# Performance work log

Measured on AMD Instinct MI355X. Metric: run time of the kernel, lower is better.

The kernel has to match this reference:

```python
import jax, jax.numpy as jnp
import numpy as np

EMBED_DIM = 1024
NUM_HEADS = 16
HEAD_DIM = EMBED_DIM // NUM_HEADS
SCALE = HEAD_DIM ** -0.5


def setup_inputs() -> dict:
    key = jax.random.key(0)
    k1, k2, k3 = jax.random.split(key, 3)
    B, S, E = 2, 2048, EMBED_DIM
    # xavier-uniform-like init scaled down for stability
    x = jax.random.normal(k1, (B, S, E), dtype=jnp.float32)
    w_qkv = jax.random.normal(k2, (3 * E, E), dtype=jnp.float32) * (E ** -0.5)
    w_out = jax.random.normal(k3, (E, E), dtype=jnp.float32) * (E ** -0.5)
    bias_qkv = jnp.zeros((3 * E,), dtype=jnp.float32)
    bias_out = jnp.zeros((E,), dtype=jnp.float32)
    return {"x": x, "w_qkv": w_qkv, "bias_qkv": bias_qkv, "w_out": w_out, "bias_out": bias_out}


def reference(x, w_qkv, bias_qkv, w_out, bias_out):
    B, S, E = x.shape
    H, D = NUM_HEADS, HEAD_DIM
    # fused QKV projection: nn.Linear semantics -> x @ w_qkv.T + bias
    qkv = jnp.einsum('bse,fe->bsf', x, w_qkv) + bias_qkv  # [B,S,3E]
    q, k, v = jnp.split(qkv, 3, axis=-1)
    # reshape to heads
    q = q.reshape(B, S, H, D)
    k = k.reshape(B, S, H, D)
    v = v.reshape(B, S, H, D)
    # scaled dot-product attention (non-causal)
    scores = jnp.einsum('bqhd,bkhd->bhqk', q, k) * SCALE  # [B,H,S,S]
    probs = jax.nn.softmax(scores, axis=-1)
    ctx = jnp.einsum('bhqk,bkhd->bqhd', probs, v).reshape(B, S, E)
    # output projection
    out = jnp.einsum('bse,fe->bsf', ctx, w_out) + bias_out
    return out
```

## Files before the change

kernel.cpp:

```cpp
#include <hip/hip_runtime.h>
#include <hip/hip_bf16.h>


typedef __bf16 bf16_t;
typedef __bf16 bf16x4 __attribute__((ext_vector_type(4)));
typedef __bf16 bf16x8 __attribute__((ext_vector_type(8)));
typedef float f32x4 __attribute__((ext_vector_type(4)));

#define MFMA16(a, b, c) __builtin_amdgcn_mfma_f32_16x16x32_bf16(a, b, c, 0, 0, 0)

static constexpr int Bn = 2;
static constexpr int S = 2048;
static constexpr int E = 1024;
static constexpr int H = 16;
static constexpr int Dh = 64;

__device__ __forceinline__ void gl_lds16(const bf16_t* g, bf16_t* l) {
  __builtin_amdgcn_global_load_lds(
      (const __attribute__((address_space(1))) unsigned int*)g,
      (__attribute__((address_space(3))) unsigned int*)l, 16, 0, 0);
}

__device__ __forceinline__ int detect_fp32(const unsigned short* p) {
  int cnt = 0;
#pragma unroll
  for (int j = 0; j < 32; j++) {
    const int e = (p[j] >> 7) & 0xFF;
    cnt += (e > 140) ? 1 : 0;
  }
  return cnt >= 2;
}

static constexpr int G0 = 4194304 / 8;
static constexpr int G1 = G0 + 3145728 / 8;
static constexpr int G2 = G1 + 3072 / 8;
static constexpr int G3 = G2 + 1048576 / 8;
static constexpr int G4 = G3 + 1024 / 8;

__global__ void convert_all(const void* __restrict__ s0, const void* __restrict__ s1,
                            const void* __restrict__ s2, const void* __restrict__ s3,
                            const void* __restrict__ s4, bf16_t* __restrict__ dst) {
  const int fp32 = detect_fp32((const unsigned short*)s0);
  const int stride = gridDim.x * blockDim.x;
  for (int i = blockIdx.x * blockDim.x + threadIdx.x; i < G4; i += stride) {
    const void* s;
    int off;
    if (i < G0)      { s = s0; off = i; }
    else if (i < G1) { s = s1; off = i - G0; }
    else if (i < G2) { s = s2; off = i - G1; }
    else if (i < G3) { s = s3; off = i - G2; }
    else             { s = s4; off = i - G3; }
    bf16x8 o;
    if (fp32) {
      const float* sp = (const float*)s + off * 8;
#pragma unroll
      for (int j = 0; j < 8; j++) o[j] = (bf16_t)sp[j];
    } else {
      o = *((const bf16x8*)s + off);
    }
    *(bf16x8*)(dst + (size_t)i * 8) = o;
  }
}

__global__ __launch_bounds__(256) void gemm_qkv(
    const bf16_t* __restrict__ X, const bf16_t* __restrict__ W,
    const bf16_t* __restrict__ bias,
    bf16_t* __restrict__ Qo, bf16_t* __restrict__ Ko, bf16_t* __restrict__ Vo) {
  __shared__ bf16_t Alds[16 * 512];
  __shared__ bf16_t Blds[16 * 512];
  const int tid = threadIdx.x;
  const int wave = tid >> 6, lane = tid & 63;
  const int lr = lane & 15, quad = lane >> 4;
  const int wm = wave >> 1, wn = wave & 1;
  const int m0 = blockIdx.y * 128, n0 = blockIdx.x * 128;
  constexpr int Kd = 1024;

  f32x4 acc[4][4] = {};
  for (int k0 = 0; k0 < Kd; k0 += 64) {
    __syncthreads();
#pragma unroll
    for (int i = 0; i < 4; i++) {
      const int fb = wave * 4 + i;
      const int mt = fb >> 1, kc = fb & 1;
      gl_lds16(X + (size_t)(m0 + mt * 16 + lr) * Kd + k0 + kc * 32 + quad * 8,
               &Alds[fb * 512]);
      gl_lds16(W + (size_t)(n0 + mt * 16 + lr) * Kd + k0 + kc * 32 + quad * 8,
               &Blds[fb * 512]);
    }
    __syncthreads();
#pragma unroll
    for (int kc = 0; kc < 2; kc++) {
      bf16x8 af[4], bfr[4];
#pragma unroll
      for (int mt = 0; mt < 4; mt++)
        af[mt] = *(const bf16x8*)&Alds[((wm * 4 + mt) * 2 + kc) * 512 + lane * 8];
#pragma unroll
      for (int nt = 0; nt < 4; nt++)
        bfr[nt] = *(const bf16x8*)&Blds[((wn * 4 + nt) * 2 + kc) * 512 + lane * 8];
#pragma unroll
      for (int mt = 0; mt < 4; mt++)
#pragma unroll
        for (int nt = 0; nt < 4; nt++)
          acc[mt][nt] = MFMA16(af[mt], bfr[nt], acc[mt][nt]);
    }
  }

  const int m0w = m0 + wm * 64, n0w = n0 + wn * 64;
#pragma unroll
  for (int nt = 0; nt < 4; nt++) {
    const int col = n0w + nt * 16 + lr;
    const float bs = (float)bias[col];
    const int which = col >> 10;
    const int e = col & 1023;
    const int h = e >> 6, d = e & 63;
#pragma unroll
    for (int mt = 0; mt < 4; mt++) {
      const int row0 = m0w + mt * 16 + quad * 4;
      const int b = row0 >> 11, s0 = row0 & 2047;
      if (which == 2) {
        bf16x4 v4;
#pragma unroll
        for (int r = 0; r < 4; r++) v4[r] = (bf16_t)(acc[mt][nt][r] + bs);
        *(bf16x4*)&Vo[((size_t)((b * H + h) * Dh + d)) * S + s0] = v4;
      } else {
        bf16_t* dst = (which == 0) ? Qo : Ko;
#pragma unroll
        for (int r = 0; r < 4; r++)
          dst[((size_t)((b * H + h) * S + (s0 + r))) * Dh + d] =
              (bf16_t)(acc[mt][nt][r] + bs);
      }
    }
  }
}

__global__ __launch_bounds__(256, 2) void attn_kernel(
    const bf16_t* __restrict__ Q, const bf16_t* __restrict__ K,
    const bf16_t* __restrict__ Vt, bf16_t* __restrict__ CTX) {
  __shared__ bf16_t Kl[2 * 8 * 512];
  __shared__ bf16_t Vl[2 * 8 * 512];
  __shared__ bf16_t Psh[4 * 32 * 64];

  const int tid = threadIdx.x;
  const int wave = tid >> 6, lane = tid & 63;
  const int lr = lane & 15, quad = lane >> 4;

  const int blk = blockIdx.x;
  const int bh = blk & 31;
  const int qt = blk >> 5;
  const int b = bh >> 4, h = bh & 15;

  const bf16_t* Qb = Q + (size_t)bh * S * Dh;
  const bf16_t* Kb = K + (size_t)bh * S * Dh;
  const bf16_t* Vb = Vt + (size_t)bh * Dh * S;

  const int q0 = qt * 128 + wave * 32;

  bf16x8 aq[2][2];
#pragma unroll
  for (int mt = 0; mt < 2; mt++)
#pragma unroll
    for (int kc = 0; kc < 2; kc++) {
      bf16x8 t = *(const bf16x8*)(Qb + (size_t)(q0 + mt * 16 + lr) * Dh +
                                  kc * 32 + quad * 8);
#pragma unroll
      for (int j = 0; j < 8; j++) t[j] = (bf16_t)((float)t[j] * 0.125f);
      aq[mt][kc] = t;
    }

  bf16x8 ones;
#pragma unroll
  for (int j = 0; j < 8; j++) ones[j] = (bf16_t)1.0f;

  bf16_t* pw = &Psh[wave * 32 * 64];
  const int xl = (lr & 7) << 3;

  const bf16_t* kg = Kb + (size_t)(wave * 16 + lr) * Dh + quad * 8;
  const bf16_t* vg = Vb + (size_t)(wave * 16 + lr) * S + quad * 8;

  f32x4 O[2][4] = {};
  f32x4 lacc[2] = {};

  {
    gl_lds16(kg, &Kl[(wave * 2 + 0) * 512]);
    gl_lds16(kg + 32, &Kl[(wave * 2 + 1) * 512]);
    gl_lds16(vg, &Vl[(wave * 2 + 0) * 512]);
    gl_lds16(vg + 32, &Vl[(wave * 2 + 1) * 512]);
  }
  __syncthreads();

  int buf = 0;
#pragma unroll 2
  for (int sk0 = 0; sk0 < S; sk0 += 64) {
    const int bb = buf * 4096;
    const int nb = (buf ^ 1) * 4096;

    if (sk0 + 64 < S) {
      const int skn = sk0 + 64;
      gl_lds16(kg + (size_t)skn * Dh, &Kl[nb + (wave * 2 + 0) * 512]);
      gl_lds16(kg + (size_t)skn * Dh + 32, &Kl[nb + (wave * 2 + 1) * 512]);
      gl_lds16(vg + skn, &Vl[nb + (wave * 2 + 0) * 512]);
      gl_lds16(vg + skn + 32, &Vl[nb + (wave * 2 + 1) * 512]);
    }

    f32x4 scT[2][4];
#pragma unroll
    for (int nt = 0; nt < 4; nt++) {
      const bf16x8 k0f = *(const bf16x8*)&Kl[bb + (nt * 2 + 0) * 512 + lane * 8];
      const bf16x8 k1f = *(const bf16x8*)&Kl[bb + (nt * 2 + 1) * 512 + lane * 8];
#pragma unroll
      for (int mt = 0; mt < 2; mt++) {
        f32x4 z = {};
        z = MFMA16(k0f, aq[mt][0], z);
        scT[mt][nt] = MFMA16(k1f, aq[mt][1], z);
      }
    }

    bf16x8 vf[4][2];
#pragma unroll
    for (int dt = 0; dt < 4; dt++) {
      vf[dt][0] = *(const bf16x8*)&Vl[bb + (dt * 2 + 0) * 512 + lane * 8];
      vf[dt][1] = *(const bf16x8*)&Vl[bb + (dt * 2 + 1) * 512 + lane * 8];
    }

#pragma unroll
    for (int mt = 0; mt < 2; mt++) {
      bf16_t* pr = &pw[(mt * 16 + lr) * 64];
#pragma unroll
      for (int nt = 0; nt < 4; nt++) {
        bf16x4 p4;
#pragma unroll
        for (int r = 0; r < 4; r++) p4[r] = (bf16_t)__expf(scT[mt][nt][r]);
        *(bf16x4*)&pr[(nt * 16 + quad * 4) ^ xl] = p4;
      }
    }

#pragma unroll
    for (int mt = 0; mt < 2; mt++) {
      const bf16x8 ap0 =
          *(const bf16x8*)&pw[(mt * 16 + lr) * 64 + ((quad * 8) ^ xl)];
      const bf16x8 ap1 =
          *(const bf16x8*)&pw[(mt * 16 + lr) * 64 + ((quad * 8 + 32) ^ xl)];
      lacc[mt] = MFMA16(ap0, ones, lacc[mt]);
      lacc[mt] = MFMA16(ap1, ones, lacc[mt]);
#pragma unroll
      for (int dt = 0; dt < 4; dt++) {
        O[mt][dt] = MFMA16(ap0, vf[dt][0], O[mt][dt]);
        O[mt][dt] = MFMA16(ap1, vf[dt][1], O[mt][dt]);
      }
    }

    __syncthreads();
    buf ^= 1;
  }

#pragma unroll
  for (int mt = 0; mt < 2; mt++) {
    float rl[4];
#pragma unroll
    for (int r = 0; r < 4; r++) rl[r] = 1.0f / lacc[mt][r];
#pragma unroll
    for (int dt = 0; dt < 4; dt++)
#pragma unroll
      for (int r = 0; r < 4; r++) {
        const int qrow = q0 + mt * 16 + quad * 4 + r;
        CTX[(size_t)(b * S + qrow) * E + h * 64 + dt * 16 + lr] =
            (bf16_t)(O[mt][dt][r] * rl[r]);
      }
  }
}

__global__ __launch_bounds__(256) void gemm_out(
    const bf16_t* __restrict__ X, const bf16_t* __restrict__ W,
    const bf16_t* __restrict__ bias, void* __restrict__ Out,
    const void* __restrict__ xin) {
  __shared__ bf16_t Alds[8 * 512];
  __shared__ bf16_t Blds[16 * 512];
  const int tid = threadIdx.x;
  const int wave = tid >> 6, lane = tid & 63;
  const int lr = lane & 15, quad = lane >> 4;
  const int wm = wave >> 1, wn = wave & 1;
  const int m0 = blockIdx.y * 64, n0 = blockIdx.x * 128;
  constexpr int Kd = 1024;

  f32x4 acc[2][4] = {};
  for (int k0 = 0; k0 < Kd; k0 += 64) {
    __syncthreads();
#pragma unroll
    for (int kc = 0; kc < 2; kc++)
      gl_lds16(X + (size_t)(m0 + wave * 16 + lr) * Kd + k0 + kc * 32 + quad * 8,
               &Alds[(wave * 2 + kc) * 512]);
#pragma unroll
    for (int i = 0; i < 2; i++) {
      const int nt = wave * 2 + i;
#pragma unroll
      for (int kc = 0; kc < 2; kc++)
        gl_lds16(W + (size_t)(n0 + nt * 16 + lr) * Kd + k0 + kc * 32 + quad * 8,
                 &Blds[(nt * 2 + kc) * 512]);
    }
    __syncthreads();
#pragma unroll
    for (int kc = 0; kc < 2; kc++) {
      bf16x8 af[2], bfr[4];
#pragma unroll
      for (int mt = 0; mt < 2; mt++)
        af[mt] = *(const bf16x8*)&Alds[((wm * 2 + mt) * 2 + kc) * 512 + lane * 8];
#pragma unroll
      for (int nt = 0; nt < 4; nt++)
        bfr[nt] = *(const bf16x8*)&Blds[((wn * 4 + nt) * 2 + kc) * 512 + lane * 8];
#pragma unroll
      for (int mt = 0; mt < 2; mt++)
#pragma unroll
        for (int nt = 0; nt < 4; nt++)
          acc[mt][nt] = MFMA16(af[mt], bfr[nt], acc[mt][nt]);
    }
  }

  const int fp32 = detect_fp32((const unsigned short*)xin);
  const int m0w = m0 + wm * 32, n0w = n0 + wn * 64;
#pragma unroll
  for (int nt = 0; nt < 4; nt++) {
    const int col = n0w + nt * 16 + lr;
    const float bs = (float)bias[col];
#pragma unroll
    for (int mt = 0; mt < 2; mt++) {
#pragma unroll
      for (int r = 0; r < 4; r++) {
        const int row = m0w + mt * 16 + quad * 4 + r;
        const float v = acc[mt][nt][r] + bs;
        if (fp32)
          ((float*)Out)[(size_t)row * E + col] = v;
        else
          ((bf16_t*)Out)[(size_t)row * E + col] = (bf16_t)v;
      }
    }
  }
}

extern "C" void kernel_launch(void* const* d_in, const int* in_sizes, int n_in,
                              void* d_out, int out_size, void* d_ws, size_t ws_size,
                              hipStream_t stream) {
  const void* x = d_in[0];
  const void* w_qkv = d_in[1];
  const void* b_qkv = d_in[2];
  const void* w_out = d_in[3];
  const void* b_out = d_in[4];

  bf16_t* base = (bf16_t*)d_ws;
  const int N_X = Bn * S * E;
  const int N_WQ = 3 * E * E;
  const int N_BQ = 3 * E;
  const int N_WO = E * E;
  const int N_BO = E;
  bf16_t* xb = base;
  bf16_t* wqb = xb + N_X;
  bf16_t* bqb = wqb + N_WQ;
  bf16_t* wob = bqb + N_BQ;
  bf16_t* bob = wob + N_WO;
  const size_t QKV_ELEMS = (size_t)Bn * H * S * Dh;
  bf16_t* Qw = bob + N_BO;
  bf16_t* Kw = Qw + QKV_ELEMS;
  bf16_t* Vw = Kw + QKV_ELEMS;
  bf16_t* CTXw = Vw + QKV_ELEMS;

  convert_all<<<1024, 256, 0, stream>>>(x, w_qkv, b_qkv, w_out, b_out, xb);
  gemm_qkv<<<dim3(3 * E / 128, Bn * S / 128), 256, 0, stream>>>(xb, wqb, bqb, Qw, Kw, Vw);
  attn_kernel<<<16 * Bn * H, 256, 0, stream>>>(Qw, Kw, Vw, CTXw);
  gemm_out<<<dim3(E / 128, Bn * S / 64), 256, 0, stream>>>(CTXw, wob, bob, d_out, x);
}
```

Baseline: 213.4 us.

## Double-buffer LDS tiles in QKV and output projection GEMMs

Both projection GEMMs now keep two LDS buffers and issue the global-to-LDS loads for the next K-tile before computing on the current one, with one barrier per iteration instead of two. The goal is to hide global load latency behind MFMA work. LDS usage per block doubles, which may lower occupancy. Correctness depends on the compiler placing a wait for the async direct-to-LDS loads before the barrier.

```diff
diff --git a/kernel.cpp b/kernel.cpp
--- a/kernel.cpp
+++ b/kernel.cpp
@@ -66,8 +66,8 @@
     const bf16_t* __restrict__ X, const bf16_t* __restrict__ W,
     const bf16_t* __restrict__ bias,
     bf16_t* __restrict__ Qo, bf16_t* __restrict__ Ko, bf16_t* __restrict__ Vo) {
-  __shared__ bf16_t Alds[16 * 512];
-  __shared__ bf16_t Blds[16 * 512];
+  __shared__ bf16_t Alds[2 * 16 * 512];
+  __shared__ bf16_t Blds[2 * 16 * 512];
   const int tid = threadIdx.x;
   const int wave = tid >> 6, lane = tid & 63;
   const int lr = lane & 15, quad = lane >> 4;
@@ -75,34 +75,45 @@
   const int m0 = blockIdx.y * 128, n0 = blockIdx.x * 128;
   constexpr int Kd = 1024;
 
-  f32x4 acc[4][4] = {};
-  for (int k0 = 0; k0 < Kd; k0 += 64) {
-    __syncthreads();
+  auto STAGE = [&](int bo, int k0) {
 #pragma unroll
     for (int i = 0; i < 4; i++) {
       const int fb = wave * 4 + i;
       const int mt = fb >> 1, kc = fb & 1;
       gl_lds16(X + (size_t)(m0 + mt * 16 + lr) * Kd + k0 + kc * 32 + quad * 8,
-               &Alds[fb * 512]);
+               &Alds[bo + fb * 512]);
       gl_lds16(W + (size_t)(n0 + mt * 16 + lr) * Kd + k0 + kc * 32 + quad * 8,
-               &Blds[fb * 512]);
-    }
-    __syncthreads();
+               &Blds[bo + fb * 512]);
+    }
+  };
+
+  f32x4 acc[4][4] = {};
+
+  STAGE(0, 0);
+  __syncthreads();
+
+  int buf = 0;
+#pragma unroll 2
+  for (int k0 = 0; k0 < Kd; k0 += 64) {
+    const int bo = buf * 8192, nbo = (buf ^ 1) * 8192;
+    if (k0 + 64 < Kd) STAGE(nbo, k0 + 64);
 #pragma unroll
     for (int kc = 0; kc < 2; kc++) {
       bf16x8 af[4], bfr[4];
 #pragma unroll
       for (int mt = 0; mt < 4; mt++)
-        af[mt] = *(const bf16x8*)&Alds[((wm * 4 + mt) * 2 + kc) * 512 + lane * 8];
+        af[mt] = *(const bf16x8*)&Alds[bo + ((wm * 4 + mt) * 2 + kc) * 512 + lane * 8];
 #pragma unroll
       for (int nt = 0; nt < 4; nt++)
-        bfr[nt] = *(const bf16x8*)&Blds[((wn * 4 + nt) * 2 + kc) * 512 + lane * 8];
+        bfr[nt] = *(const bf16x8*)&Blds[bo + ((wn * 4 + nt) * 2 + kc) * 512 + lane * 8];
 #pragma unroll
       for (int mt = 0; mt < 4; mt++)
 #pragma unroll
         for (int nt = 0; nt < 4; nt++)
           acc[mt][nt] = MFMA16(af[mt], bfr[nt], acc[mt][nt]);
     }
+    __syncthreads();
+    buf ^= 1;
   }
 
   const int m0w = m0 + wm * 64, n0w = n0 + wn * 64;
@@ -273,8 +284,8 @@
     const bf16_t* __restrict__ X, const bf16_t* __restrict__ W,
     const bf16_t* __restrict__ bias, void* __restrict__ Out,
     const void* __restrict__ xin) {
-  __shared__ bf16_t Alds[8 * 512];
-  __shared__ bf16_t Blds[16 * 512];
+  __shared__ bf16_t Alds[2 * 8 * 512];
+  __shared__ bf16_t Blds[2 * 16 * 512];
   const int tid = threadIdx.x;
   const int wave = tid >> 6, lane = tid & 63;
   const int lr = lane & 15, quad = lane >> 4;
@@ -282,37 +293,48 @@
   const int m0 = blockIdx.y * 64, n0 = blockIdx.x * 128;
   constexpr int Kd = 1024;
 
-  f32x4 acc[2][4] = {};
-  for (int k0 = 0; k0 < Kd; k0 += 64) {
-    __syncthreads();
+  auto STAGE = [&](int ao, int bo, int k0) {
 #pragma unroll
     for (int kc = 0; kc < 2; kc++)
       gl_lds16(X + (size_t)(m0 + wave * 16 + lr) * Kd + k0 + kc * 32 + quad * 8,
-               &Alds[(wave * 2 + kc) * 512]);
+               &Alds[ao + (wave * 2 + kc) * 512]);
 #pragma unroll
     for (int i = 0; i < 2; i++) {
       const int nt = wave * 2 + i;
 #pragma unroll
       for (int kc = 0; kc < 2; kc++)
         gl_lds16(W + (size_t)(n0 + nt * 16 + lr) * Kd + k0 + kc * 32 + quad * 8,
-                 &Blds[(nt * 2 + kc) * 512]);
-    }
-    __syncthreads();
+                 &Blds[bo + (nt * 2 + kc) * 512]);
+    }
+  };
+
+  f32x4 acc[2][4] = {};
+
+  STAGE(0, 0, 0);
+  __syncthreads();
+
+  int buf = 0;
+#pragma unroll 2
+  for (int k0 = 0; k0 < Kd; k0 += 64) {
+    const int ao = buf * 4096, bo = buf * 8192;
+    if (k0 + 64 < Kd) STAGE(ao ^ 4096, bo ^ 8192, k0 + 64);
 #pragma unroll
     for (int kc = 0; kc < 2; kc++) {
       bf16x8 af[2], bfr[4];
 #pragma unroll
       for (int mt = 0; mt < 2; mt++)
-        af[mt] = *(const bf16x8*)&Alds[((wm * 2 + mt) * 2 + kc) * 512 + lane * 8];
+        af[mt] = *(const bf16x8*)&Alds[ao + ((wm * 2 + mt) * 2 + kc) * 512 + lane * 8];
 #pragma unroll
       for (int nt = 0; nt < 4; nt++)
-        bfr[nt] = *(const bf16x8*)&Blds[((wn * 4 + nt) * 2 + kc) * 512 + lane * 8];
+        bfr[nt] = *(const bf16x8*)&Blds[bo + ((wn * 4 + nt) * 2 + kc) * 512 + lane * 8];
 #pragma unroll
       for (int mt = 0; mt < 2; mt++)
 #pragma unroll
         for (int nt = 0; nt < 4; nt++)
           acc[mt][nt] = MFMA16(af[mt], bfr[nt], acc[mt][nt]);
     }
+    __syncthreads();
+    buf ^= 1;
   }
 
   const int fp32 = detect_fp32((const unsigned short*)xin);
```

Measured after the change: 225.0 us. +5.4%, slower.
